# Kernel tuning notes

Measured on AMD Instinct MI355X. Metric: run time of the kernel, lower is better.

Reference implementation:

```python
import jax, jax.numpy as jnp
import numpy as np

N_HEADS = 16
WINDOW = 512  # sliding_window_size
D_MODEL = 1024


def setup_inputs() -> dict:
    key = jax.random.key(0)
    ks = jax.random.split(key, 5)
    d = D_MODEL
    x = jax.random.normal(ks[0], (2, 2048, d), dtype=jnp.float32)
    # nn.Linear(d, d, bias=False): weight shape [d_out, d_in], y = x @ W.T
    s = 1.0 / np.sqrt(d)
    Wq = jax.random.uniform(ks[1], (d, d), jnp.float32, -s, s)
    Wk = jax.random.uniform(ks[2], (d, d), jnp.float32, -s, s)
    Wv = jax.random.uniform(ks[3], (d, d), jnp.float32, -s, s)
    Wo = jax.random.uniform(ks[4], (d, d), jnp.float32, -s, s)
    return {"x": x, "Wq": Wq, "Wk": Wk, "Wv": Wv, "Wo": Wo}


def reference(x, Wq, Wk, Wv, Wo):
    B, T, C = x.shape
    H = N_HEADS
    hd = C // H
    # QKV projections -> [B, H, T, hd]
    def proj(W):
        return (x @ W.T).reshape(B, T, H, hd).transpose(0, 2, 1, 3)
    q, k, v = proj(Wq), proj(Wk), proj(Wv)
    # Sliding-window mask (module sets is_causal=False in this branch):
    # row i attends to j in [max(0,i-w+1), min(T,i+w)) i.e. |i-j| <= w-1
    idx = jnp.arange(T)
    mask = jnp.abs(idx[:, None] - idx[None, :]) < WINDOW  # [T, T] bool
    scale = 1.0 / np.sqrt(hd)
    scores = jnp.einsum("bhqd,bhkd->bhqk", q, k) * scale  # [B,H,T,T]
    neg = jnp.asarray(jnp.finfo(scores.dtype).min, scores.dtype)
    scores = jnp.where(mask, scores, neg)
    attn = jax.nn.softmax(scores, axis=-1)
    y = jnp.einsum("bhqk,bhkd->bhqd", attn, v)  # [B,H,T,hd]
    y = y.transpose(0, 2, 1, 3).reshape(B, T, C)
    return y @ Wo.T
```

## Files before the change

### kernel.cpp

```cpp
#include <hip/hip_runtime.h>

#define BATCH 2
#define TSEQ  2048
#define CDIM  1024
#define NH    16
#define HD    64
#define WIN   512
#define MROWS (BATCH * TSEQ)

typedef __attribute__((ext_vector_type(8))) short short8;
typedef __attribute__((ext_vector_type(4))) float f32x4;

static __device__ __forceinline__ unsigned short f2bf(float f) {
    union { float f; unsigned u; } v; v.f = f;
    unsigned r = v.u + 0x7FFFu + ((v.u >> 16) & 1u);
    return (unsigned short)(r >> 16);
}

static __device__ __forceinline__ f32x4 mfma16(short8 a, short8 b, f32x4 c) {
    return __builtin_amdgcn_mfma_f32_16x16x32_bf16(a, b, c, 0, 0, 0);
}

__global__ __launch_bounds__(256) void convert_inputs(
    const float* __restrict__ x,  const float* __restrict__ wq,
    const float* __restrict__ wk, const float* __restrict__ wv,
    const float* __restrict__ wo,
    unsigned short* __restrict__ xb,  unsigned short* __restrict__ wqb,
    unsigned short* __restrict__ wkb, unsigned short* __restrict__ wvb,
    unsigned short* __restrict__ wob)
{
    const long i8 = (long)(blockIdx.x * 256 + threadIdx.x) * 8;
    const long XN = (long)MROWS * CDIM;
    const long WN = (long)CDIM * CDIM;
    const float* src; unsigned short* dst; long off;
    if (i8 < XN) { src = x; dst = xb; off = i8; }
    else {
        long j = i8 - XN; int w = (int)(j / WN); off = j - (long)w * WN;
        src = (w == 0) ? wq : (w == 1) ? wk : (w == 2) ? wv : wo;
        dst = (w == 0) ? wqb : (w == 1) ? wkb : (w == 2) ? wvb : wob;
    }
    const float4 a = *(const float4*)&src[off];
    const float4 b = *(const float4*)&src[off + 4];
    uint4 o;
    o.x = f2bf(a.x) | ((unsigned)f2bf(a.y) << 16);
    o.y = f2bf(a.z) | ((unsigned)f2bf(a.w) << 16);
    o.z = f2bf(b.x) | ((unsigned)f2bf(b.y) << 16);
    o.w = f2bf(b.z) | ((unsigned)f2bf(b.w) << 16);
    *(uint4*)&dst[off] = o;
}

template <int MODE>
__global__ __launch_bounds__(256) void gemm_bf16(
    const unsigned short* __restrict__ A,
    const unsigned short* __restrict__ W0, const unsigned short* __restrict__ W1,
    const unsigned short* __restrict__ W2,
    void* __restrict__ O0, void* __restrict__ O1, void* __restrict__ O2)
{
    constexpr int KD = CDIM;
    __shared__ unsigned short As[128][40];
    __shared__ unsigned short Bs[128][40];

    const int tid  = threadIdx.x;
    const int lane = tid & 63;
    const int w    = tid >> 6;
    const int wm   = (w >> 1) * 64;
    const int wn   = (w & 1) * 64;
    const int m0   = blockIdx.x * 128;
    const int n0   = blockIdx.y * 128;
    const unsigned short* Wm = (blockIdx.z == 0) ? W0 : (blockIdx.z == 1) ? W1 : W2;

    const int r0  = tid >> 2;
    const int ch0 = (tid & 3) * 8;
    const unsigned short* gA0 = A  + (size_t)(m0 + r0) * KD + ch0;
    const unsigned short* gA1 = gA0 + (size_t)64 * KD;
    const unsigned short* gB0 = Wm + (size_t)(n0 + r0) * KD + ch0;
    const unsigned short* gB1 = gB0 + (size_t)64 * KD;

    const f32x4 fz = {0.f, 0.f, 0.f, 0.f};
    f32x4 acc[4][4];
#pragma unroll
    for (int i = 0; i < 4; ++i)
#pragma unroll
        for (int j = 0; j < 4; ++j) acc[i][j] = fz;

    uint4 ra0 = *(const uint4*)gA0;
    uint4 ra1 = *(const uint4*)gA1;
    uint4 rb0 = *(const uint4*)gB0;
    uint4 rb1 = *(const uint4*)gB1;

    const int fr = lane & 15;
    const int fc = (lane >> 4) * 8;

    for (int kt = 0; kt < KD / 32; ++kt) {
        if (kt) __syncthreads();
        *(uint4*)&As[r0][ch0]      = ra0;
        *(uint4*)&As[r0 + 64][ch0] = ra1;
        *(uint4*)&Bs[r0][ch0]      = rb0;
        *(uint4*)&Bs[r0 + 64][ch0] = rb1;
        __syncthreads();
        if (kt + 1 < KD / 32) {
            const int ko = (kt + 1) * 32;
            ra0 = *(const uint4*)(gA0 + ko);
            ra1 = *(const uint4*)(gA1 + ko);
            rb0 = *(const uint4*)(gB0 + ko);
            rb1 = *(const uint4*)(gB1 + ko);
        }
        short8 af[4], bf[4];
#pragma unroll
        for (int mt = 0; mt < 4; ++mt)
            af[mt] = *(const short8*)&As[wm + mt * 16 + fr][fc];
#pragma unroll
        for (int nt = 0; nt < 4; ++nt)
            bf[nt] = *(const short8*)&Bs[wn + nt * 16 + fr][fc];
#pragma unroll
        for (int mt = 0; mt < 4; ++mt)
#pragma unroll
            for (int nt = 0; nt < 4; ++nt)
                acc[mt][nt] = mfma16(af[mt], bf[nt], acc[mt][nt]);
    }

    const int fg = lane >> 4;
    if constexpr (MODE == 0) {
        float* Out = (float*)O0;
#pragma unroll
        for (int mt = 0; mt < 4; ++mt) {
            const int row0 = m0 + wm + mt * 16 + fg * 4;
#pragma unroll
            for (int nt = 0; nt < 4; ++nt) {
                const int col = n0 + wn + nt * 16 + fr;
#pragma unroll
                for (int r = 0; r < 4; ++r)
                    Out[(size_t)(row0 + r) * CDIM + col] = acc[mt][nt][r];
            }
        }
    } else {
        unsigned short* Out = (unsigned short*)((blockIdx.z == 0) ? O0 : (blockIdx.z == 1) ? O1 : O2);
        const bool vmode = (blockIdx.z == 2);
#pragma unroll
        for (int mt = 0; mt < 4; ++mt) {
            const int row0 = m0 + wm + mt * 16 + fg * 4;
            const int b  = row0 >> 11;
            const int t0 = row0 & (TSEQ - 1);
#pragma unroll
            for (int nt = 0; nt < 4; ++nt) {
                const int col = n0 + wn + nt * 16 + fr;
                const int h = col >> 6, d = col & 63;
                if (!vmode) {
#pragma unroll
                    for (int r = 0; r < 4; ++r)
                        Out[(((size_t)b * NH + h) * TSEQ + (t0 + r)) * HD + d] =
                            f2bf(acc[mt][nt][r]);
                } else {
                    ushort4 pk;
                    pk.x = f2bf(acc[mt][nt][0]); pk.y = f2bf(acc[mt][nt][1]);
                    pk.z = f2bf(acc[mt][nt][2]); pk.w = f2bf(acc[mt][nt][3]);
                    *(ushort4*)&Out[(((size_t)b * NH + h) * HD + d) * TSEQ + t0] = pk;
                }
            }
        }
    }
}

__global__ __launch_bounds__(256) void attn_mfma(
    const unsigned short* __restrict__ Qg, const unsigned short* __restrict__ Kg,
    const unsigned short* __restrict__ Vg, unsigned short* __restrict__ Y)
{
    __shared__ unsigned short Ks[64][72];
    __shared__ unsigned short Vs[64][72];
    __shared__ unsigned short Ps[4][16][72];

    const int tid  = threadIdx.x;
    const int lane = tid & 63;
    const int w    = tid >> 6;
    const int q0   = blockIdx.x * 64;
    const int bh   = blockIdx.y;

    const unsigned short* Qb = Qg + (size_t)bh * TSEQ * HD;
    const unsigned short* Kb = Kg + (size_t)bh * TSEQ * HD;
    const unsigned short* Vb = Vg + (size_t)bh * HD * TSEQ;

    const int fr = lane & 15;
    const int fg = lane >> 4;

    const short8 qa0 = *(const short8*)&Qb[(size_t)(q0 + w * 16 + fr) * HD + fg * 8];
    const short8 qa1 = *(const short8*)&Qb[(size_t)(q0 + w * 16 + fr) * HD + 32 + fg * 8];

    const f32x4 fz = {0.f, 0.f, 0.f, 0.f};
    f32x4 Oacc[4];
    float mrow[4], lsum[4];
#pragma unroll
    for (int i = 0; i < 4; ++i) { Oacc[i] = fz; mrow[i] = -1e30f; lsum[i] = 0.f; }

    int kbeg = q0 - (WIN - 1); if (kbeg < 0) kbeg = 0; kbeg &= ~63;
    int kend = q0 + 64 + (WIN - 1); if (kend > TSEQ) kend = TSEQ;

    const int sr = tid >> 3;
    const int sc = (tid & 7) * 8;
    uint4 kreg0 = *(const uint4*)&Kb[(size_t)(kbeg + sr) * HD + sc];
    uint4 kreg1 = *(const uint4*)&Kb[(size_t)(kbeg + sr + 32) * HD + sc];
    uint4 vreg0 = *(const uint4*)&Vb[(size_t)sr * TSEQ + kbeg + sc];
    uint4 vreg1 = *(const uint4*)&Vb[(size_t)(sr + 32) * TSEQ + kbeg + sc];

    const float scale = 0.125f;

    for (int k0 = kbeg; k0 < kend; k0 += 64) {
        if (k0 != kbeg) __syncthreads();
        *(uint4*)&Ks[sr][sc]      = kreg0;
        *(uint4*)&Ks[sr + 32][sc] = kreg1;
        *(uint4*)&Vs[sr][sc]      = vreg0;
        *(uint4*)&Vs[sr + 32][sc] = vreg1;
        __syncthreads();
        if (k0 + 64 < kend) {
            kreg0 = *(const uint4*)&Kb[(size_t)(k0 + 64 + sr) * HD + sc];
            kreg1 = *(const uint4*)&Kb[(size_t)(k0 + 96 + sr) * HD + sc];
            vreg0 = *(const uint4*)&Vb[(size_t)sr * TSEQ + k0 + 64 + sc];
            vreg1 = *(const uint4*)&Vb[(size_t)(sr + 32) * TSEQ + k0 + 64 + sc];
        }

        f32x4 S[4];
#pragma unroll
        for (int nt = 0; nt < 4; ++nt) {
            const short8 kb0 = *(const short8*)&Ks[nt * 16 + fr][fg * 8];
            const short8 kb1 = *(const short8*)&Ks[nt * 16 + fr][32 + fg * 8];
            f32x4 s = fz;
            s = mfma16(qa0, kb0, s);
            s = mfma16(qa1, kb1, s);
            S[nt] = s;
        }

        float p[4][4], fsc[4];
#pragma unroll
        for (int r = 0; r < 4; ++r) {
            const int irow = q0 + w * 16 + fg * 4 + r;
            float sv[4];
            float mx = -1e30f;
#pragma unroll
            for (int nt = 0; nt < 4; ++nt) {
                const int jcol = k0 + nt * 16 + fr;
                const bool ok = (unsigned)(irow - jcol + (WIN - 1)) < (unsigned)(2 * WIN - 1);
                const float v = ok ? S[nt][r] * scale : -1e30f;
                sv[nt] = v;
                mx = fmaxf(mx, v);
            }
#pragma unroll
            for (int o = 1; o < 16; o <<= 1) mx = fmaxf(mx, __shfl_xor(mx, o, 16));
            const float mnew = fmaxf(mrow[r], mx);
            const float f = __expf(mrow[r] - mnew);
            float ps = 0.f;
#pragma unroll
            for (int nt = 0; nt < 4; ++nt) {
                const float pv = (sv[nt] > -1e29f) ? __expf(sv[nt] - mnew) : 0.f;
                p[r][nt] = pv; ps += pv;
            }
#pragma unroll
            for (int o = 1; o < 16; o <<= 1) ps += __shfl_xor(ps, o, 16);
            lsum[r] = lsum[r] * f + ps;
            mrow[r] = mnew;
            fsc[r]  = f;
        }
#pragma unroll
        for (int db = 0; db < 4; ++db) {
            f32x4 t = Oacc[db];
            t[0] *= fsc[0]; t[1] *= fsc[1]; t[2] *= fsc[2]; t[3] *= fsc[3];
            Oacc[db] = t;
        }

#pragma unroll
        for (int r = 0; r < 4; ++r)
#pragma unroll
            for (int nt = 0; nt < 4; ++nt)
                Ps[w][fg * 4 + r][nt * 16 + fr] = f2bf(p[r][nt]);

        const short8 pa0 = *(const short8*)&Ps[w][fr][fg * 8];
        const short8 pa1 = *(const short8*)&Ps[w][fr][32 + fg * 8];
#pragma unroll
        for (int db = 0; db < 4; ++db) {
            const short8 vb0 = *(const short8*)&Vs[db * 16 + fr][fg * 8];
            const short8 vb1 = *(const short8*)&Vs[db * 16 + fr][32 + fg * 8];
            Oacc[db] = mfma16(pa0, vb0, Oacc[db]);
            Oacc[db] = mfma16(pa1, vb1, Oacc[db]);
        }
    }

    const int b = bh >> 4, h = bh & 15;
    float inv[4];
#pragma unroll
    for (int r = 0; r < 4; ++r) inv[r] = 1.f / lsum[r];
#pragma unroll
    for (int db = 0; db < 4; ++db)
#pragma unroll
        for (int r = 0; r < 4; ++r) {
            const int t = q0 + w * 16 + fg * 4 + r;
            Y[(size_t)(b * TSEQ + t) * CDIM + h * HD + db * 16 + fr] =
                f2bf(Oacc[db][r] * inv[r]);
        }
}

extern "C" void kernel_launch(void* const* d_in, const int* in_sizes, int n_in,
                              void* d_out, int out_size, void* d_ws, size_t ws_size,
                              hipStream_t stream)
{
    const float* x  = (const float*)d_in[0];
    const float* Wq = (const float*)d_in[1];
    const float* Wk = (const float*)d_in[2];
    const float* Wv = (const float*)d_in[3];
    const float* Wo = (const float*)d_in[4];
    float* out = (float*)d_out;

    const size_t XN = (size_t)MROWS * CDIM;
    const size_t WN = (size_t)CDIM * CDIM;
    unsigned short* xb  = (unsigned short*)d_ws;
    unsigned short* wqb = xb  + XN;
    unsigned short* wkb = wqb + WN;
    unsigned short* wvb = wkb + WN;
    unsigned short* wob = wvb + WN;
    unsigned short* Qb  = wob + WN;
    unsigned short* Kb  = Qb  + XN;
    unsigned short* Vb  = Kb  + XN;
    unsigned short* Yb  = Vb  + XN;

    convert_inputs<<<dim3(4096), 256, 0, stream>>>(x, Wq, Wk, Wv, Wo,
                                                   xb, wqb, wkb, wvb, wob);
    gemm_bf16<1><<<dim3(MROWS / 128, CDIM / 128, 3), 256, 0, stream>>>(
        xb, wqb, wkb, wvb, Qb, Kb, Vb);
    attn_mfma<<<dim3(TSEQ / 64, BATCH * NH), 256, 0, stream>>>(Qb, Kb, Vb, Yb);
    gemm_bf16<0><<<dim3(MROWS / 128, CDIM / 128, 1), 256, 0, stream>>>(
        Yb, wob, wob, wob, out, out, out);
}
```

Measured before the change: 207.2 us.

## Fuse fp32-to-bf16 conversion into GEMM loads and enlarge attention query blocks

Removes the separate input conversion kernel: the GEMMs now load fp32 x and weights directly and pack them to bf16 in registers with v_cvt_pk_bf16_f32. This drops a launch and the extra round trip through workspace, but every GEMM block now re-reads and re-converts fp32 data, doubling global load bytes. The attention kernel moves to 128-query blocks with 32 rows per wave, computes S transposed, skips mask arithmetic on fully in-window tiles, folds the softmax scale into the Q projection epilogue, and swizzles block order across heads for locality.

New measurement: 200.2 us. 1.04x faster.

```diff
diff --git a/kernel.cpp b/kernel.cpp
--- a/kernel.cpp
+++ b/kernel.cpp
@@ -7,6 +7,7 @@
 #define HD    64
 #define WIN   512
 #define MROWS (BATCH * TSEQ)
+#define QBLK  128
 
 typedef __attribute__((ext_vector_type(8))) short short8;
 typedef __attribute__((ext_vector_type(4))) float f32x4;
@@ -17,43 +18,36 @@
     return (unsigned short)(r >> 16);
 }
 
+static __device__ __forceinline__ unsigned cvtpk(float a, float b) {
+    unsigned r;
+    asm("v_cvt_pk_bf16_f32 %0, %1, %2" : "=v"(r) : "v"(a), "v"(b));
+    return r;
+}
+
 static __device__ __forceinline__ f32x4 mfma16(short8 a, short8 b, f32x4 c) {
     return __builtin_amdgcn_mfma_f32_16x16x32_bf16(a, b, c, 0, 0, 0);
 }
 
-__global__ __launch_bounds__(256) void convert_inputs(
-    const float* __restrict__ x,  const float* __restrict__ wq,
-    const float* __restrict__ wk, const float* __restrict__ wv,
-    const float* __restrict__ wo,
-    unsigned short* __restrict__ xb,  unsigned short* __restrict__ wqb,
-    unsigned short* __restrict__ wkb, unsigned short* __restrict__ wvb,
-    unsigned short* __restrict__ wob)
-{
-    const long i8 = (long)(blockIdx.x * 256 + threadIdx.x) * 8;
-    const long XN = (long)MROWS * CDIM;
-    const long WN = (long)CDIM * CDIM;
-    const float* src; unsigned short* dst; long off;
-    if (i8 < XN) { src = x; dst = xb; off = i8; }
-    else {
-        long j = i8 - XN; int w = (int)(j / WN); off = j - (long)w * WN;
-        src = (w == 0) ? wq : (w == 1) ? wk : (w == 2) ? wv : wo;
-        dst = (w == 0) ? wqb : (w == 1) ? wkb : (w == 2) ? wvb : wob;
-    }
-    const float4 a = *(const float4*)&src[off];
-    const float4 b = *(const float4*)&src[off + 4];
-    uint4 o;
-    o.x = f2bf(a.x) | ((unsigned)f2bf(a.y) << 16);
-    o.y = f2bf(a.z) | ((unsigned)f2bf(a.w) << 16);
-    o.z = f2bf(b.x) | ((unsigned)f2bf(b.y) << 16);
-    o.w = f2bf(b.z) | ((unsigned)f2bf(b.w) << 16);
-    *(uint4*)&dst[off] = o;
-}
-
-template <int MODE>
+template <int F32>
+static __device__ __forceinline__ uint4 ld8(const void* p, size_t eoff) {
+    if constexpr (F32) {
+        const float* f = (const float*)p + eoff;
+        const float4 a = *(const float4*)f;
+        const float4 b = *(const float4*)(f + 4);
+        uint4 o;
+        o.x = cvtpk(a.x, a.y); o.y = cvtpk(a.z, a.w);
+        o.z = cvtpk(b.x, b.y); o.w = cvtpk(b.z, b.w);
+        return o;
+    } else {
+        return *(const uint4*)((const unsigned short*)p + eoff);
+    }
+}
+
+template <int MODE, int AF32, int WF32>
 __global__ __launch_bounds__(256) void gemm_bf16(
-    const unsigned short* __restrict__ A,
-    const unsigned short* __restrict__ W0, const unsigned short* __restrict__ W1,
-    const unsigned short* __restrict__ W2,
+    const void* __restrict__ A,
+    const void* __restrict__ W0, const void* __restrict__ W1,
+    const void* __restrict__ W2,
     void* __restrict__ O0, void* __restrict__ O1, void* __restrict__ O2)
 {
     constexpr int KD = CDIM;
@@ -67,14 +61,14 @@
     const int wn   = (w & 1) * 64;
     const int m0   = blockIdx.x * 128;
     const int n0   = blockIdx.y * 128;
-    const unsigned short* Wm = (blockIdx.z == 0) ? W0 : (blockIdx.z == 1) ? W1 : W2;
+    const void* Wm = (blockIdx.z == 0) ? W0 : (blockIdx.z == 1) ? W1 : W2;
 
     const int r0  = tid >> 2;
     const int ch0 = (tid & 3) * 8;
-    const unsigned short* gA0 = A  + (size_t)(m0 + r0) * KD + ch0;
-    const unsigned short* gA1 = gA0 + (size_t)64 * KD;
-    const unsigned short* gB0 = Wm + (size_t)(n0 + r0) * KD + ch0;
-    const unsigned short* gB1 = gB0 + (size_t)64 * KD;
+    const size_t aoff0 = (size_t)(m0 + r0) * KD + ch0;
+    const size_t aoff1 = aoff0 + (size_t)64 * KD;
+    const size_t boff0 = (size_t)(n0 + r0) * KD + ch0;
+    const size_t boff1 = boff0 + (size_t)64 * KD;
 
     const f32x4 fz = {0.f, 0.f, 0.f, 0.f};
     f32x4 acc[4][4];
@@ -83,10 +77,10 @@
 #pragma unroll
         for (int j = 0; j < 4; ++j) acc[i][j] = fz;
 
-    uint4 ra0 = *(const uint4*)gA0;
-    uint4 ra1 = *(const uint4*)gA1;
-    uint4 rb0 = *(const uint4*)gB0;
-    uint4 rb1 = *(const uint4*)gB1;
+    uint4 ra0 = ld8<AF32>(A, aoff0);
+    uint4 ra1 = ld8<AF32>(A, aoff1);
+    uint4 rb0 = ld8<WF32>(Wm, boff0);
+    uint4 rb1 = ld8<WF32>(Wm, boff1);
 
     const int fr = lane & 15;
     const int fc = (lane >> 4) * 8;
@@ -100,10 +94,10 @@
         __syncthreads();
         if (kt + 1 < KD / 32) {
             const int ko = (kt + 1) * 32;
-            ra0 = *(const uint4*)(gA0 + ko);
-            ra1 = *(const uint4*)(gA1 + ko);
-            rb0 = *(const uint4*)(gB0 + ko);
-            rb1 = *(const uint4*)(gB1 + ko);
+            ra0 = ld8<AF32>(A, aoff0 + ko);
+            ra1 = ld8<AF32>(A, aoff1 + ko);
+            rb0 = ld8<WF32>(Wm, boff0 + ko);
+            rb1 = ld8<WF32>(Wm, boff1 + ko);
         }
         short8 af[4], bf[4];
 #pragma unroll
@@ -136,6 +130,7 @@
     } else {
         unsigned short* Out = (unsigned short*)((blockIdx.z == 0) ? O0 : (blockIdx.z == 1) ? O1 : O2);
         const bool vmode = (blockIdx.z == 2);
+        const float qs = (blockIdx.z == 0) ? 0.125f : 1.0f;
 #pragma unroll
         for (int mt = 0; mt < 4; ++mt) {
             const int row0 = m0 + wm + mt * 16 + fg * 4;
@@ -149,7 +144,7 @@
 #pragma unroll
                     for (int r = 0; r < 4; ++r)
                         Out[(((size_t)b * NH + h) * TSEQ + (t0 + r)) * HD + d] =
-                            f2bf(acc[mt][nt][r]);
+                            f2bf(acc[mt][nt][r] * qs);
                 } else {
                     ushort4 pk;
                     pk.x = f2bf(acc[mt][nt][0]); pk.y = f2bf(acc[mt][nt][1]);
@@ -167,13 +162,16 @@
 {
     __shared__ unsigned short Ks[64][72];
     __shared__ unsigned short Vs[64][72];
-    __shared__ unsigned short Ps[4][16][72];
+    __shared__ unsigned short Ps[4][32][72];
 
     const int tid  = threadIdx.x;
     const int lane = tid & 63;
     const int w    = tid >> 6;
-    const int q0   = blockIdx.x * 64;
-    const int bh   = blockIdx.y;
+
+    const int blk = blockIdx.x;
+    const int wg  = (blk & 7) * 64 + (blk >> 3);
+    const int bh  = wg >> 4;
+    const int q0  = (wg & 15) * QBLK;
 
     const unsigned short* Qb = Qg + (size_t)bh * TSEQ * HD;
     const unsigned short* Kb = Kg + (size_t)bh * TSEQ * HD;
@@ -182,17 +180,27 @@
     const int fr = lane & 15;
     const int fg = lane >> 4;
 
-    const short8 qa0 = *(const short8*)&Qb[(size_t)(q0 + w * 16 + fr) * HD + fg * 8];
-    const short8 qa1 = *(const short8*)&Qb[(size_t)(q0 + w * 16 + fr) * HD + 32 + fg * 8];
+    const int wq0 = q0 + w * 32;
+
+    short8 qa[2][2];
+#pragma unroll
+    for (int mt = 0; mt < 2; ++mt)
+#pragma unroll
+        for (int kh = 0; kh < 2; ++kh)
+            qa[mt][kh] = *(const short8*)&Qb[(size_t)(wq0 + mt * 16 + fr) * HD + kh * 32 + fg * 8];
 
     const f32x4 fz = {0.f, 0.f, 0.f, 0.f};
-    f32x4 Oacc[4];
-    float mrow[4], lsum[4];
-#pragma unroll
-    for (int i = 0; i < 4; ++i) { Oacc[i] = fz; mrow[i] = -1e30f; lsum[i] = 0.f; }
+    f32x4 Oacc[2][4];
+    float mrow[2], lsum[2];
+#pragma unroll
+    for (int mt = 0; mt < 2; ++mt) {
+        mrow[mt] = -1e30f; lsum[mt] = 0.f;
+#pragma unroll
+        for (int dt = 0; dt < 4; ++dt) Oacc[mt][dt] = fz;
+    }
 
     int kbeg = q0 - (WIN - 1); if (kbeg < 0) kbeg = 0; kbeg &= ~63;
-    int kend = q0 + 64 + (WIN - 1); if (kend > TSEQ) kend = TSEQ;
+    int kend = q0 + QBLK + (WIN - 1); if (kend > TSEQ) kend = TSEQ;
 
     const int sr = tid >> 3;
     const int sc = (tid & 7) * 8;
@@ -200,8 +208,6 @@
     uint4 kreg1 = *(const uint4*)&Kb[(size_t)(kbeg + sr + 32) * HD + sc];
     uint4 vreg0 = *(const uint4*)&Vb[(size_t)sr * TSEQ + kbeg + sc];
     uint4 vreg1 = *(const uint4*)&Vb[(size_t)(sr + 32) * TSEQ + kbeg + sc];
-
-    const float scale = 0.125f;
 
     for (int k0 = kbeg; k0 < kend; k0 += 64) {
         if (k0 != kbeg) __syncthreads();
@@ -217,83 +223,112 @@
             vreg1 = *(const uint4*)&Vb[(size_t)(sr + 32) * TSEQ + k0 + 64 + sc];
         }
 
-        f32x4 S[4];
-#pragma unroll
-        for (int nt = 0; nt < 4; ++nt) {
-            const short8 kb0 = *(const short8*)&Ks[nt * 16 + fr][fg * 8];
-            const short8 kb1 = *(const short8*)&Ks[nt * 16 + fr][32 + fg * 8];
-            f32x4 s = fz;
-            s = mfma16(qa0, kb0, s);
-            s = mfma16(qa1, kb1, s);
-            S[nt] = s;
-        }
-
-        float p[4][4], fsc[4];
-#pragma unroll
-        for (int r = 0; r < 4; ++r) {
-            const int irow = q0 + w * 16 + fg * 4 + r;
-            float sv[4];
-            float mx = -1e30f;
-#pragma unroll
-            for (int nt = 0; nt < 4; ++nt) {
-                const int jcol = k0 + nt * 16 + fr;
-                const bool ok = (unsigned)(irow - jcol + (WIN - 1)) < (unsigned)(2 * WIN - 1);
-                const float v = ok ? S[nt][r] * scale : -1e30f;
-                sv[nt] = v;
-                mx = fmaxf(mx, v);
-            }
-#pragma unroll
-            for (int o = 1; o < 16; o <<= 1) mx = fmaxf(mx, __shfl_xor(mx, o, 16));
-            const float mnew = fmaxf(mrow[r], mx);
-            const float f = __expf(mrow[r] - mnew);
-            float ps = 0.f;
-#pragma unroll
-            for (int nt = 0; nt < 4; ++nt) {
-                const float pv = (sv[nt] > -1e29f) ? __expf(sv[nt] - mnew) : 0.f;
-                p[r][nt] = pv; ps += pv;
-            }
-#pragma unroll
-            for (int o = 1; o < 16; o <<= 1) ps += __shfl_xor(ps, o, 16);
-            lsum[r] = lsum[r] * f + ps;
-            mrow[r] = mnew;
-            fsc[r]  = f;
-        }
-#pragma unroll
-        for (int db = 0; db < 4; ++db) {
-            f32x4 t = Oacc[db];
-            t[0] *= fsc[0]; t[1] *= fsc[1]; t[2] *= fsc[2]; t[3] *= fsc[3];
-            Oacc[db] = t;
-        }
-
-#pragma unroll
-        for (int r = 0; r < 4; ++r)
-#pragma unroll
-            for (int nt = 0; nt < 4; ++nt)
-                Ps[w][fg * 4 + r][nt * 16 + fr] = f2bf(p[r][nt]);
-
-        const short8 pa0 = *(const short8*)&Ps[w][fr][fg * 8];
-        const short8 pa1 = *(const short8*)&Ps[w][fr][32 + fg * 8];
-#pragma unroll
-        for (int db = 0; db < 4; ++db) {
-            const short8 vb0 = *(const short8*)&Vs[db * 16 + fr][fg * 8];
-            const short8 vb1 = *(const short8*)&Vs[db * 16 + fr][32 + fg * 8];
-            Oacc[db] = mfma16(pa0, vb0, Oacc[db]);
-            Oacc[db] = mfma16(pa1, vb1, Oacc[db]);
+        short8 ka[4][2];
+#pragma unroll
+        for (int kt = 0; kt < 4; ++kt)
+#pragma unroll
+            for (int kh = 0; kh < 2; ++kh)
+                ka[kt][kh] = *(const short8*)&Ks[kt * 16 + fr][kh * 32 + fg * 8];
+
+        f32x4 S[2][4];
+#pragma unroll
+        for (int mt = 0; mt < 2; ++mt)
+#pragma unroll
+            for (int kt = 0; kt < 4; ++kt) {
+                f32x4 s = fz;
+                s = mfma16(ka[kt][0], qa[mt][0], s);
+                s = mfma16(ka[kt][1], qa[mt][1], s);
+                S[mt][kt] = s;
+            }
+
+        const bool full = (k0 >= q0 - 384) && (k0 <= q0 + 448);
+
+#pragma unroll
+        for (int mt = 0; mt < 2; ++mt) {
+            const int q = wq0 + mt * 16 + fr;
+            float sv[16];
+#pragma unroll
+            for (int kt = 0; kt < 4; ++kt)
+#pragma unroll
+                for (int r = 0; r < 4; ++r) {
+                    float v = S[mt][kt][r];
+                    if (!full) {
+                        const int key = k0 + kt * 16 + fg * 4 + r;
+                        const bool ok = (unsigned)(q - key + (WIN - 1)) < (unsigned)(2 * WIN - 1);
+                        v = ok ? v : -1e30f;
+                    }
+                    sv[kt * 4 + r] = v;
+                }
+            float mx = sv[0];
+#pragma unroll
+            for (int i = 1; i < 16; ++i) mx = fmaxf(mx, sv[i]);
+            mx = fmaxf(mx, __shfl_xor(mx, 16));
+            mx = fmaxf(mx, __shfl_xor(mx, 32));
+            const float mnew = fmaxf(mrow[mt], mx);
+            const float f = __expf(mrow[mt] - mnew);
+            float p[16], ps = 0.f;
+            if (full) {
+#pragma unroll
+                for (int i = 0; i < 16; ++i) { p[i] = __expf(sv[i] - mnew); ps += p[i]; }
+            } else {
+#pragma unroll
+                for (int i = 0; i < 16; ++i) {
+                    p[i] = (sv[i] > -1e29f) ? __expf(sv[i] - mnew) : 0.f;
+                    ps += p[i];
+                }
+            }
+            ps += __shfl_xor(ps, 16);
+            ps += __shfl_xor(ps, 32);
+            lsum[mt] = lsum[mt] * f + ps;
+            mrow[mt] = mnew;
+#pragma unroll
+            for (int dt = 0; dt < 4; ++dt) {
+                f32x4 t = Oacc[mt][dt];
+                t[0] *= f; t[1] *= f; t[2] *= f; t[3] *= f;
+                Oacc[mt][dt] = t;
+            }
+#pragma unroll
+            for (int kt = 0; kt < 4; ++kt) {
+                ushort4 pk;
+                pk.x = f2bf(p[kt * 4 + 0]); pk.y = f2bf(p[kt * 4 + 1]);
+                pk.z = f2bf(p[kt * 4 + 2]); pk.w = f2bf(p[kt * 4 + 3]);
+                *(ushort4*)&Ps[w][mt * 16 + fr][kt * 16 + fg * 4] = pk;
+            }
+        }
+
+#pragma unroll
+        for (int kh = 0; kh < 2; ++kh) {
+            short8 pb[2], va[4];
+#pragma unroll
+            for (int mt = 0; mt < 2; ++mt)
+                pb[mt] = *(const short8*)&Ps[w][mt * 16 + fr][kh * 32 + fg * 8];
+#pragma unroll
+            for (int dt = 0; dt < 4; ++dt)
+                va[dt] = *(const short8*)&Vs[dt * 16 + fr][kh * 32 + fg * 8];
+#pragma unroll
+            for (int mt = 0; mt < 2; ++mt)
+#pragma unroll
+                for (int dt = 0; dt < 4; ++dt)
+                    Oacc[mt][dt] = mfma16(va[dt], pb[mt], Oacc[mt][dt]);
         }
     }
 
     const int b = bh >> 4, h = bh & 15;
-    float inv[4];
-#pragma unroll
-    for (int r = 0; r < 4; ++r) inv[r] = 1.f / lsum[r];
-#pragma unroll
-    for (int db = 0; db < 4; ++db)
-#pragma unroll
-        for (int r = 0; r < 4; ++r) {
-            const int t = q0 + w * 16 + fg * 4 + r;
-            Y[(size_t)(b * TSEQ + t) * CDIM + h * HD + db * 16 + fr] =
-                f2bf(Oacc[db][r] * inv[r]);
-        }
+#pragma unroll
+    for (int mt = 0; mt < 2; ++mt) {
+        const float inv = 1.f / lsum[mt];
+        const int t = wq0 + mt * 16 + fr;
+        unsigned short* dst = &Y[(size_t)(b * TSEQ + t) * CDIM + h * HD];
+#pragma unroll
+        for (int dt = 0; dt < 4; ++dt) {
+            ushort4 pk;
+            pk.x = f2bf(Oacc[mt][dt][0] * inv);
+            pk.y = f2bf(Oacc[mt][dt][1] * inv);
+            pk.z = f2bf(Oacc[mt][dt][2] * inv);
+            pk.w = f2bf(Oacc[mt][dt][3] * inv);
+            *(ushort4*)&dst[dt * 16 + fg * 4] = pk;
+        }
+    }
 }
 
 extern "C" void kernel_launch(void* const* d_in, const int* in_sizes, int n_in,
@@ -308,22 +343,14 @@
     float* out = (float*)d_out;
 
     const size_t XN = (size_t)MROWS * CDIM;
-    const size_t WN = (size_t)CDIM * CDIM;
-    unsigned short* xb  = (unsigned short*)d_ws;
-    unsigned short* wqb = xb  + XN;
-    unsigned short* wkb = wqb + WN;
-    unsigned short* wvb = wkb + WN;
-    unsigned short* wob = wvb + WN;
-    unsigned short* Qb  = wob + WN;
-    unsigned short* Kb  = Qb  + XN;
-    unsigned short* Vb  = Kb  + XN;
-    unsigned short* Yb  = Vb  + XN;
-
-    convert_inputs<<<dim3(4096), 256, 0, stream>>>(x, Wq, Wk, Wv, Wo,
-                                                   xb, wqb, wkb, wvb, wob);
-    gemm_bf16<1><<<dim3(MROWS / 128, CDIM / 128, 3), 256, 0, stream>>>(
-        xb, wqb, wkb, wvb, Qb, Kb, Vb);
-    attn_mfma<<<dim3(TSEQ / 64, BATCH * NH), 256, 0, stream>>>(Qb, Kb, Vb, Yb);
-    gemm_bf16<0><<<dim3(MROWS / 128, CDIM / 128, 1), 256, 0, stream>>>(
-        Yb, wob, wob, wob, out, out, out);
-}
+    unsigned short* Qb = (unsigned short*)d_ws;
+    unsigned short* Kb = Qb + XN;
+    unsigned short* Vb = Kb + XN;
+    unsigned short* Yb = Vb + XN;
+
+    gemm_bf16<1, 1, 1><<<dim3(MROWS / 128, CDIM / 128, 3), 256, 0, stream>>>(
+        x, Wq, Wk, Wv, Qb, Kb, Vb);
+    attn_mfma<<<dim3((TSEQ / QBLK) * BATCH * NH), 256, 0, stream>>>(Qb, Kb, Vb, Yb);
+    gemm_bf16<0, 0, 1><<<dim3(MROWS / 128, CDIM / 128, 1), 256, 0, stream>>>(
+        Yb, Wo, Wo, Wo, out, out, out);
+}
```

## Use direct-to-LDS swizzled GEMM loads and restructure attention with larger query blocks

Applied to the files above, without the earlier changes.

The GEMM now loads tiles straight into shared memory with global_load_lds into an XOR-swizzled layout, replacing the register-staged copies, and the Q projection is pre-scaled by 1/sqrt(hd). The attention kernel moves to 128-query blocks with 512 threads, so each K/V tile serves more queries. It computes S transposed so each lane owns one query row, which drops most cross-lane shuffles, and it skips masking for tiles fully inside the window. Blocks are remapped for locality and Y is written with vector stores. The GEMM change removes the register round-trip but leaves one shared buffer with two barriers per k-step, so global latency is less hidden.

After: 182.3 us. 1.14x faster.

```diff
diff --git a/kernel.cpp b/kernel.cpp
--- a/kernel.cpp
+++ b/kernel.cpp
@@ -7,6 +7,7 @@
 #define HD    64
 #define WIN   512
 #define MROWS (BATCH * TSEQ)
+#define QBLK  128
 
 typedef __attribute__((ext_vector_type(8))) short short8;
 typedef __attribute__((ext_vector_type(4))) float f32x4;
@@ -19,6 +20,12 @@
 
 static __device__ __forceinline__ f32x4 mfma16(short8 a, short8 b, f32x4 c) {
     return __builtin_amdgcn_mfma_f32_16x16x32_bf16(a, b, c, 0, 0, 0);
+}
+
+static __device__ __forceinline__ void gld16(const void* g, void* l) {
+    __builtin_amdgcn_global_load_lds(
+        (const __attribute__((address_space(1))) unsigned int*)g,
+        (__attribute__((address_space(3))) unsigned int*)l, 16, 0, 0);
 }
 
 __global__ __launch_bounds__(256) void convert_inputs(
@@ -57,8 +64,8 @@
     void* __restrict__ O0, void* __restrict__ O1, void* __restrict__ O2)
 {
     constexpr int KD = CDIM;
-    __shared__ unsigned short As[128][40];
-    __shared__ unsigned short Bs[128][40];
+    __shared__ unsigned short As[128 * 32];
+    __shared__ unsigned short Bs[128 * 32];
 
     const int tid  = threadIdx.x;
     const int lane = tid & 63;
@@ -69,12 +76,23 @@
     const int n0   = blockIdx.y * 128;
     const unsigned short* Wm = (blockIdx.z == 0) ? W0 : (blockIdx.z == 1) ? W1 : W2;
 
-    const int r0  = tid >> 2;
-    const int ch0 = (tid & 3) * 8;
-    const unsigned short* gA0 = A  + (size_t)(m0 + r0) * KD + ch0;
-    const unsigned short* gA1 = gA0 + (size_t)64 * KD;
-    const unsigned short* gB0 = Wm + (size_t)(n0 + r0) * KD + ch0;
-    const unsigned short* gB1 = gB0 + (size_t)64 * KD;
+    const int srow = w * 16 + (lane >> 2);
+    const int sch  = (lane & 3) ^ ((srow >> 1) & 3);
+    const unsigned short* gA = A  + (size_t)(m0 + srow) * KD + sch * 8;
+    const unsigned short* gB = Wm + (size_t)(n0 + srow) * KD + sch * 8;
+    unsigned short* lA = As + (size_t)(w * 16) * 32;
+    unsigned short* lB = Bs + (size_t)(w * 16) * 32;
+
+    const int fr = lane & 15;
+    const int fg = lane >> 4;
+    int aoff[4], boff[4];
+#pragma unroll
+    for (int i = 0; i < 4; ++i) {
+        const int Ra = wm + i * 16 + fr;
+        aoff[i] = Ra * 32 + (fg ^ ((Ra >> 1) & 3)) * 8;
+        const int Rb = wn + i * 16 + fr;
+        boff[i] = Rb * 32 + (fg ^ ((Rb >> 1) & 3)) * 8;
+    }
 
     const f32x4 fz = {0.f, 0.f, 0.f, 0.f};
     f32x4 acc[4][4];
@@ -83,48 +101,35 @@
 #pragma unroll
         for (int j = 0; j < 4; ++j) acc[i][j] = fz;
 
-    uint4 ra0 = *(const uint4*)gA0;
-    uint4 ra1 = *(const uint4*)gA1;
-    uint4 rb0 = *(const uint4*)gB0;
-    uint4 rb1 = *(const uint4*)gB1;
-
-    const int fr = lane & 15;
-    const int fc = (lane >> 4) * 8;
+    gld16(gA, lA);  gld16(gA + (size_t)64 * KD, lA + 64 * 32);
+    gld16(gB, lB);  gld16(gB + (size_t)64 * KD, lB + 64 * 32);
 
     for (int kt = 0; kt < KD / 32; ++kt) {
-        if (kt) __syncthreads();
-        *(uint4*)&As[r0][ch0]      = ra0;
-        *(uint4*)&As[r0 + 64][ch0] = ra1;
-        *(uint4*)&Bs[r0][ch0]      = rb0;
-        *(uint4*)&Bs[r0 + 64][ch0] = rb1;
         __syncthreads();
-        if (kt + 1 < KD / 32) {
-            const int ko = (kt + 1) * 32;
-            ra0 = *(const uint4*)(gA0 + ko);
-            ra1 = *(const uint4*)(gA1 + ko);
-            rb0 = *(const uint4*)(gB0 + ko);
-            rb1 = *(const uint4*)(gB1 + ko);
-        }
         short8 af[4], bf[4];
 #pragma unroll
-        for (int mt = 0; mt < 4; ++mt)
-            af[mt] = *(const short8*)&As[wm + mt * 16 + fr][fc];
-#pragma unroll
-        for (int nt = 0; nt < 4; ++nt)
-            bf[nt] = *(const short8*)&Bs[wn + nt * 16 + fr][fc];
+        for (int mt = 0; mt < 4; ++mt) af[mt] = *(const short8*)&As[aoff[mt]];
+#pragma unroll
+        for (int nt = 0; nt < 4; ++nt) bf[nt] = *(const short8*)&Bs[boff[nt]];
 #pragma unroll
         for (int mt = 0; mt < 4; ++mt)
 #pragma unroll
             for (int nt = 0; nt < 4; ++nt)
                 acc[mt][nt] = mfma16(af[mt], bf[nt], acc[mt][nt]);
-    }
-
-    const int fg = lane >> 4;
+        if (kt + 1 < KD / 32) {
+            __syncthreads();
+            const int ko = (kt + 1) * 32;
+            gld16(gA + ko, lA);  gld16(gA + ko + (size_t)64 * KD, lA + 64 * 32);
+            gld16(gB + ko, lB);  gld16(gB + ko + (size_t)64 * KD, lB + 64 * 32);
+        }
+    }
+
+    const int fgr = lane >> 4;
     if constexpr (MODE == 0) {
         float* Out = (float*)O0;
 #pragma unroll
         for (int mt = 0; mt < 4; ++mt) {
-            const int row0 = m0 + wm + mt * 16 + fg * 4;
+            const int row0 = m0 + wm + mt * 16 + fgr * 4;
 #pragma unroll
             for (int nt = 0; nt < 4; ++nt) {
                 const int col = n0 + wn + nt * 16 + fr;
@@ -136,9 +141,10 @@
     } else {
         unsigned short* Out = (unsigned short*)((blockIdx.z == 0) ? O0 : (blockIdx.z == 1) ? O1 : O2);
         const bool vmode = (blockIdx.z == 2);
+        const float qs = (blockIdx.z == 0) ? 0.125f : 1.0f;
 #pragma unroll
         for (int mt = 0; mt < 4; ++mt) {
-            const int row0 = m0 + wm + mt * 16 + fg * 4;
+            const int row0 = m0 + wm + mt * 16 + fgr * 4;
             const int b  = row0 >> 11;
             const int t0 = row0 & (TSEQ - 1);
 #pragma unroll
@@ -149,7 +155,7 @@
 #pragma unroll
                     for (int r = 0; r < 4; ++r)
                         Out[(((size_t)b * NH + h) * TSEQ + (t0 + r)) * HD + d] =
-                            f2bf(acc[mt][nt][r]);
+                            f2bf(acc[mt][nt][r] * qs);
                 } else {
                     ushort4 pk;
                     pk.x = f2bf(acc[mt][nt][0]); pk.y = f2bf(acc[mt][nt][1]);
@@ -161,19 +167,22 @@
     }
 }
 
-__global__ __launch_bounds__(256) void attn_mfma(
+__global__ __launch_bounds__(512, 4) void attn_mfma(
     const unsigned short* __restrict__ Qg, const unsigned short* __restrict__ Kg,
     const unsigned short* __restrict__ Vg, unsigned short* __restrict__ Y)
 {
     __shared__ unsigned short Ks[64][72];
     __shared__ unsigned short Vs[64][72];
-    __shared__ unsigned short Ps[4][16][72];
+    __shared__ unsigned short Ps[8][16][72];
 
     const int tid  = threadIdx.x;
     const int lane = tid & 63;
     const int w    = tid >> 6;
-    const int q0   = blockIdx.x * 64;
-    const int bh   = blockIdx.y;
+
+    const int blk = blockIdx.x;
+    const int wg  = (blk & 7) * 64 + (blk >> 3);
+    const int bh  = wg >> 4;
+    const int q0  = (wg & 15) * QBLK;
 
     const unsigned short* Qb = Qg + (size_t)bh * TSEQ * HD;
     const unsigned short* Kb = Kg + (size_t)bh * TSEQ * HD;
@@ -181,119 +190,131 @@
 
     const int fr = lane & 15;
     const int fg = lane >> 4;
-
-    const short8 qa0 = *(const short8*)&Qb[(size_t)(q0 + w * 16 + fr) * HD + fg * 8];
-    const short8 qa1 = *(const short8*)&Qb[(size_t)(q0 + w * 16 + fr) * HD + 32 + fg * 8];
+    const int wq0 = q0 + w * 16;
+
+    short8 qa[2];
+#pragma unroll
+    for (int kh = 0; kh < 2; ++kh)
+        qa[kh] = *(const short8*)&Qb[(size_t)(wq0 + fr) * HD + kh * 32 + fg * 8];
 
     const f32x4 fz = {0.f, 0.f, 0.f, 0.f};
     f32x4 Oacc[4];
-    float mrow[4], lsum[4];
-#pragma unroll
-    for (int i = 0; i < 4; ++i) { Oacc[i] = fz; mrow[i] = -1e30f; lsum[i] = 0.f; }
+    float mrow = -1e30f, lsum = 0.f;
+#pragma unroll
+    for (int dt = 0; dt < 4; ++dt) Oacc[dt] = fz;
 
     int kbeg = q0 - (WIN - 1); if (kbeg < 0) kbeg = 0; kbeg &= ~63;
-    int kend = q0 + 64 + (WIN - 1); if (kend > TSEQ) kend = TSEQ;
+    int kend = q0 + QBLK + (WIN - 1); if (kend > TSEQ) kend = TSEQ;
 
     const int sr = tid >> 3;
     const int sc = (tid & 7) * 8;
-    uint4 kreg0 = *(const uint4*)&Kb[(size_t)(kbeg + sr) * HD + sc];
-    uint4 kreg1 = *(const uint4*)&Kb[(size_t)(kbeg + sr + 32) * HD + sc];
-    uint4 vreg0 = *(const uint4*)&Vb[(size_t)sr * TSEQ + kbeg + sc];
-    uint4 vreg1 = *(const uint4*)&Vb[(size_t)(sr + 32) * TSEQ + kbeg + sc];
-
-    const float scale = 0.125f;
+    uint4 kreg = *(const uint4*)&Kb[(size_t)(kbeg + sr) * HD + sc];
+    uint4 vreg = *(const uint4*)&Vb[(size_t)sr * TSEQ + kbeg + sc];
 
     for (int k0 = kbeg; k0 < kend; k0 += 64) {
         if (k0 != kbeg) __syncthreads();
-        *(uint4*)&Ks[sr][sc]      = kreg0;
-        *(uint4*)&Ks[sr + 32][sc] = kreg1;
-        *(uint4*)&Vs[sr][sc]      = vreg0;
-        *(uint4*)&Vs[sr + 32][sc] = vreg1;
+        *(uint4*)&Ks[sr][sc] = kreg;
+        *(uint4*)&Vs[sr][sc] = vreg;
         __syncthreads();
         if (k0 + 64 < kend) {
-            kreg0 = *(const uint4*)&Kb[(size_t)(k0 + 64 + sr) * HD + sc];
-            kreg1 = *(const uint4*)&Kb[(size_t)(k0 + 96 + sr) * HD + sc];
-            vreg0 = *(const uint4*)&Vb[(size_t)sr * TSEQ + k0 + 64 + sc];
-            vreg1 = *(const uint4*)&Vb[(size_t)(sr + 32) * TSEQ + k0 + 64 + sc];
-        }
+            kreg = *(const uint4*)&Kb[(size_t)(k0 + 64 + sr) * HD + sc];
+            vreg = *(const uint4*)&Vb[(size_t)sr * TSEQ + k0 + 64 + sc];
+        }
+
+        short8 ka[4][2];
+#pragma unroll
+        for (int kt = 0; kt < 4; ++kt)
+#pragma unroll
+            for (int kh = 0; kh < 2; ++kh)
+                ka[kt][kh] = *(const short8*)&Ks[kt * 16 + fr][kh * 32 + fg * 8];
 
         f32x4 S[4];
 #pragma unroll
-        for (int nt = 0; nt < 4; ++nt) {
-            const short8 kb0 = *(const short8*)&Ks[nt * 16 + fr][fg * 8];
-            const short8 kb1 = *(const short8*)&Ks[nt * 16 + fr][32 + fg * 8];
+        for (int kt = 0; kt < 4; ++kt) {
             f32x4 s = fz;
-            s = mfma16(qa0, kb0, s);
-            s = mfma16(qa1, kb1, s);
-            S[nt] = s;
-        }
-
-        float p[4][4], fsc[4];
-#pragma unroll
-        for (int r = 0; r < 4; ++r) {
-            const int irow = q0 + w * 16 + fg * 4 + r;
-            float sv[4];
-            float mx = -1e30f;
-#pragma unroll
-            for (int nt = 0; nt < 4; ++nt) {
-                const int jcol = k0 + nt * 16 + fr;
-                const bool ok = (unsigned)(irow - jcol + (WIN - 1)) < (unsigned)(2 * WIN - 1);
-                const float v = ok ? S[nt][r] * scale : -1e30f;
-                sv[nt] = v;
-                mx = fmaxf(mx, v);
+            s = mfma16(ka[kt][0], qa[0], s);
+            s = mfma16(ka[kt][1], qa[1], s);
+            S[kt] = s;
+        }
+
+        const bool full = (k0 >= q0 - 384) && (k0 <= q0 + 448);
+
+        const int q = wq0 + fr;
+        float sv[16];
+#pragma unroll
+        for (int kt = 0; kt < 4; ++kt)
+#pragma unroll
+            for (int r = 0; r < 4; ++r) {
+                float v = S[kt][r];
+                if (!full) {
+                    const int key = k0 + kt * 16 + fg * 4 + r;
+                    const bool ok = (unsigned)(q - key + (WIN - 1)) < (unsigned)(2 * WIN - 1);
+                    v = ok ? v : -1e30f;
+                }
+                sv[kt * 4 + r] = v;
             }
-#pragma unroll
-            for (int o = 1; o < 16; o <<= 1) mx = fmaxf(mx, __shfl_xor(mx, o, 16));
-            const float mnew = fmaxf(mrow[r], mx);
-            const float f = __expf(mrow[r] - mnew);
-            float ps = 0.f;
-#pragma unroll
-            for (int nt = 0; nt < 4; ++nt) {
-                const float pv = (sv[nt] > -1e29f) ? __expf(sv[nt] - mnew) : 0.f;
-                p[r][nt] = pv; ps += pv;
+        float mx = sv[0];
+#pragma unroll
+        for (int i = 1; i < 16; ++i) mx = fmaxf(mx, sv[i]);
+        mx = fmaxf(mx, __shfl_xor(mx, 16));
+        mx = fmaxf(mx, __shfl_xor(mx, 32));
+        const float mnew = fmaxf(mrow, mx);
+        const float f = __expf(mrow - mnew);
+        float p[16], ps = 0.f;
+        if (full) {
+#pragma unroll
+            for (int i = 0; i < 16; ++i) { p[i] = __expf(sv[i] - mnew); ps += p[i]; }
+        } else {
+#pragma unroll
+            for (int i = 0; i < 16; ++i) {
+                p[i] = (sv[i] > -1e29f) ? __expf(sv[i] - mnew) : 0.f;
+                ps += p[i];
             }
-#pragma unroll
-            for (int o = 1; o < 16; o <<= 1) ps += __shfl_xor(ps, o, 16);
-            lsum[r] = lsum[r] * f + ps;
-            mrow[r] = mnew;
-            fsc[r]  = f;
-        }
-#pragma unroll
-        for (int db = 0; db < 4; ++db) {
-            f32x4 t = Oacc[db];
-            t[0] *= fsc[0]; t[1] *= fsc[1]; t[2] *= fsc[2]; t[3] *= fsc[3];
-            Oacc[db] = t;
-        }
-
-#pragma unroll
-        for (int r = 0; r < 4; ++r)
-#pragma unroll
-            for (int nt = 0; nt < 4; ++nt)
-                Ps[w][fg * 4 + r][nt * 16 + fr] = f2bf(p[r][nt]);
-
-        const short8 pa0 = *(const short8*)&Ps[w][fr][fg * 8];
-        const short8 pa1 = *(const short8*)&Ps[w][fr][32 + fg * 8];
-#pragma unroll
-        for (int db = 0; db < 4; ++db) {
-            const short8 vb0 = *(const short8*)&Vs[db * 16 + fr][fg * 8];
-            const short8 vb1 = *(const short8*)&Vs[db * 16 + fr][32 + fg * 8];
-            Oacc[db] = mfma16(pa0, vb0, Oacc[db]);
-            Oacc[db] = mfma16(pa1, vb1, Oacc[db]);
+        }
+        ps += __shfl_xor(ps, 16);
+        ps += __shfl_xor(ps, 32);
+        lsum = lsum * f + ps;
+        mrow = mnew;
+#pragma unroll
+        for (int dt = 0; dt < 4; ++dt) {
+            f32x4 t = Oacc[dt];
+            t[0] *= f; t[1] *= f; t[2] *= f; t[3] *= f;
+            Oacc[dt] = t;
+        }
+#pragma unroll
+        for (int kt = 0; kt < 4; ++kt) {
+            ushort4 pk;
+            pk.x = f2bf(p[kt * 4 + 0]); pk.y = f2bf(p[kt * 4 + 1]);
+            pk.z = f2bf(p[kt * 4 + 2]); pk.w = f2bf(p[kt * 4 + 3]);
+            *(ushort4*)&Ps[w][fr][kt * 16 + fg * 4] = pk;
+        }
+
+#pragma unroll
+        for (int kh = 0; kh < 2; ++kh) {
+            const short8 pb = *(const short8*)&Ps[w][fr][kh * 32 + fg * 8];
+            short8 va[4];
+#pragma unroll
+            for (int dt = 0; dt < 4; ++dt)
+                va[dt] = *(const short8*)&Vs[dt * 16 + fr][kh * 32 + fg * 8];
+#pragma unroll
+            for (int dt = 0; dt < 4; ++dt)
+                Oacc[dt] = mfma16(va[dt], pb, Oacc[dt]);
         }
     }
 
     const int b = bh >> 4, h = bh & 15;
-    float inv[4];
-#pragma unroll
-    for (int r = 0; r < 4; ++r) inv[r] = 1.f / lsum[r];
-#pragma unroll
-    for (int db = 0; db < 4; ++db)
-#pragma unroll
-        for (int r = 0; r < 4; ++r) {
-            const int t = q0 + w * 16 + fg * 4 + r;
-            Y[(size_t)(b * TSEQ + t) * CDIM + h * HD + db * 16 + fr] =
-                f2bf(Oacc[db][r] * inv[r]);
-        }
+    const float inv = 1.f / lsum;
+    const int t = wq0 + fr;
+    unsigned short* dst = &Y[(size_t)(b * TSEQ + t) * CDIM + h * HD];
+#pragma unroll
+    for (int dt = 0; dt < 4; ++dt) {
+        ushort4 pk;
+        pk.x = f2bf(Oacc[dt][0] * inv);
+        pk.y = f2bf(Oacc[dt][1] * inv);
+        pk.z = f2bf(Oacc[dt][2] * inv);
+        pk.w = f2bf(Oacc[dt][3] * inv);
+        *(ushort4*)&dst[dt * 16 + fg * 4] = pk;
+    }
 }
 
 extern "C" void kernel_launch(void* const* d_in, const int* in_sizes, int n_in,
@@ -323,7 +344,7 @@
                                                    xb, wqb, wkb, wvb, wob);
     gemm_bf16<1><<<dim3(MROWS / 128, CDIM / 128, 3), 256, 0, stream>>>(
         xb, wqb, wkb, wvb, Qb, Kb, Vb);
-    attn_mfma<<<dim3(TSEQ / 64, BATCH * NH), 256, 0, stream>>>(Qb, Kb, Vb, Yb);
+    attn_mfma<<<dim3((TSEQ / QBLK) * BATCH * NH), 512, 0, stream>>>(Qb, Kb, Vb, Yb);
     gemm_bf16<0><<<dim3(MROWS / 128, CDIM / 128, 1), 256, 0, stream>>>(
         Yb, wob, wob, wob, out, out, out);
 }
```
